# Kernel optimization log

Hardware: AMD Instinct MI355X
Metric: run time of the kernel (lower is better)

## Reference

```python
import jax, jax.numpy as jnp
import numpy as np

BLANK = 0


def setup_inputs() -> dict:
    key = jax.random.key(0)
    k1, k2 = jax.random.split(key)
    B, T, V = 64, 4096, 128
    feature = jax.random.normal(k1, (B, T, V), dtype=jnp.float32)
    lengths = jax.random.randint(k2, (B,), 1, T + 1, dtype=jnp.int32)
    return {"feature": feature, "lengths": lengths, "beam_width": 1}


def reference(feature, lengths, beam_width):
    # Greedy CTC decode (beam_width <= 1 path of the torch module), fully vectorized.
    # feature: (B, T, V) raw logits; lengths: (B,) valid frame counts.
    B, T, V = feature.shape
    logp = jax.nn.log_softmax(feature.astype(jnp.float32), axis=-1)  # (B, T, V)
    max_scores = jnp.max(logp, axis=-1)                               # (B, T)
    tokens = jnp.argmax(logp, axis=-1).astype(jnp.int32)              # (B, T)

    tmask = jnp.arange(T)[None, :] < lengths[:, None]                 # (B, T) valid frames
    logp_scores = jnp.sum(jnp.where(tmask, max_scores, 0.0), axis=-1) # (B,)

    # CTC collapse: keep token iff it is not blank and differs from previous frame's token.
    # (t != prev or prev == blank) and t != blank  ==  (t != blank) and (t != prev)
    prev = jnp.concatenate(
        [jnp.full((B, 1), BLANK, dtype=tokens.dtype), tokens[:, :-1]], axis=1
    )
    keep = (tokens != BLANK) & (tokens != prev) & tmask               # (B, T)

    # Fixed-shape encoding of the ragged prediction lists:
    # tokens[b, t] is part of prediction[b] (in time order) wherever keep[b, t].
    return tokens, keep, logp_scores
```

## Files before the change

### kernel.cpp

```cpp
#include <hip/hip_runtime.h>

#define BLANK 0

__global__ __launch_bounds__(256) void ctc_rowmax(const float* __restrict__ feat,
                                                  const int* __restrict__ lengths,
                                                  float* __restrict__ out_tok,
                                                  float* __restrict__ partial,
                                                  int npairs, int Tshift, int Tmask)
{
    const int lane = threadIdx.x & 63;
    const int l32  = lane & 31;
    const int half = lane >> 5;
    const int wid  = (blockIdx.x * 256 + (int)threadIdx.x) >> 6;
    const int nw   = (gridDim.x * 256) >> 6;
    const int nquads = npairs >> 2;

    for (int q = wid; q < nquads; q += nw) {
        const int pair0 = q << 2;
        const float4* base = (const float4*)feat + (size_t)pair0 * 64;
        float4 v0 = base[lane];
        float4 v1 = base[64 + lane];
        float4 v2 = base[128 + lane];
        float4 v3 = base[192 + lane];

        const int row0 = pair0 << 1;
        const int len  = lengths[row0 >> Tshift];
        float acc = 0.0f;

        auto process = [&](float4 v, int pair) {
            float m = v.x; int li = 0;
            if (v.y > m) { m = v.y; li = 1; }
            if (v.z > m) { m = v.z; li = 2; }
            if (v.w > m) { m = v.w; li = 3; }
            const float lm  = m;
            const int  lidx = (l32 << 2) + li;
            float s = __expf(v.x) + __expf(v.y) + __expf(v.z) + __expf(v.w);
            #pragma unroll
            for (int off = 16; off >= 1; off >>= 1) {
                m  = fmaxf(m, __shfl_xor(m, off, 64));
                s += __shfl_xor(s, off, 64);
            }
            unsigned long long bal = __ballot(lm == m);
            unsigned seg = half ? (unsigned)(bal >> 32) : (unsigned)bal;
            int src = (__ffs(seg) - 1) | (half << 5);
            int idx = __shfl(lidx, src, 64);
            const int row = (pair << 1) + half;
            if (l32 == 0) {
                out_tok[row] = (float)idx;
                if ((row & Tmask) < len) acc += m - __logf(s);
            }
        };
        process(v0, pair0);
        process(v1, pair0 + 1);
        process(v2, pair0 + 2);
        process(v3, pair0 + 3);

        acc += __shfl_xor(acc, 32, 64);
        if (lane == 0) partial[row0 >> 3] = acc;
    }
}

__global__ __launch_bounds__(256) void ctc_collapse(const int* __restrict__ lengths,
                                                    const float* __restrict__ out_tok,
                                                    const float* __restrict__ partial,
                                                    float* __restrict__ keep,
                                                    float* __restrict__ scores,
                                                    int T, int Tdiv8)
{
    const int b = blockIdx.y;
    const int t = blockIdx.x * 256 + (int)threadIdx.x;
    const size_t base = (size_t)b * T;
    if (t < T) {
        float tk = out_tok[base + t];
        float pv = (t == 0) ? (float)BLANK : out_tok[base + t - 1];
        bool valid = t < lengths[b];
        keep[base + t] = (tk != (float)BLANK && tk != pv && valid) ? 1.0f : 0.0f;
    }
    if (blockIdx.x == 0) {
        float s = 0.0f;
        for (int i = threadIdx.x; i < Tdiv8; i += 256)
            s += partial[(size_t)b * Tdiv8 + i];
        #pragma unroll
        for (int off = 32; off >= 1; off >>= 1) s += __shfl_xor(s, off, 64);
        __shared__ float red[4];
        if ((threadIdx.x & 63) == 0) red[threadIdx.x >> 6] = s;
        __syncthreads();
        if (threadIdx.x == 0) scores[b] = red[0] + red[1] + red[2] + red[3];
    }
}

extern "C" void kernel_launch(void* const* d_in, const int* in_sizes, int n_in,
                              void* d_out, int out_size, void* d_ws, size_t ws_size,
                              hipStream_t stream) {
    const float* feat    = (const float*)d_in[0];
    const int*   lengths = (const int*)d_in[1];

    const int V  = 128;
    const int B  = in_sizes[1];
    const int T  = in_sizes[0] / (B * V);
    const int BT = B * T;

    float* out_tok = (float*)d_out;
    float* keep    = out_tok + (size_t)BT;
    float* scores  = out_tok + (size_t)2 * BT;
    float* partial = (float*)d_ws;

    int Tshift = 31 - __builtin_clz((unsigned)T);
    int Tmask  = T - 1;
    int npairs = BT >> 1;

    ctc_rowmax<<<2048, 256, 0, stream>>>(feat, lengths, out_tok, partial,
                                         npairs, Tshift, Tmask);

    dim3 g2((T + 255) / 256, B);
    ctc_collapse<<<g2, 256, 0, stream>>>(lengths, out_tok, partial, keep, scores,
                                         T, T >> 3);
}
```

Baseline: 192.2 us.

## Remap rowmax so 8 lanes each own a row with 16 contiguous values

Each wavefront still handles 8 rows per iteration, but the work is now split as 8 lanes per row, each lane loading 4 consecutive float4s (16 columns), instead of one row per 32-lane half processed four times. This cuts the cross-lane reductions from four 5-step shuffle trees to a single 3-step tree, plus one ballot and index shuffle, which removes most shuffle and ballot overhead. The cost is that each lane's loads now have a 64-byte stride between lanes, so coalescing is worse than the previous fully contiguous float4 pattern. Each lane also holds more live registers.

```diff
diff --git a/kernel.cpp b/kernel.cpp
--- a/kernel.cpp
+++ b/kernel.cpp
@@ -6,57 +6,66 @@
                                                   const int* __restrict__ lengths,
                                                   float* __restrict__ out_tok,
                                                   float* __restrict__ partial,
-                                                  int npairs, int Tshift, int Tmask)
+                                                  int ngroups, int Tshift, int Tmask)
 {
     const int lane = threadIdx.x & 63;
-    const int l32  = lane & 31;
-    const int half = lane >> 5;
+    const int seg  = lane & 7;
+    const int r    = lane >> 3;
     const int wid  = (blockIdx.x * 256 + (int)threadIdx.x) >> 6;
     const int nw   = (gridDim.x * 256) >> 6;
-    const int nquads = npairs >> 2;
 
-    for (int q = wid; q < nquads; q += nw) {
-        const int pair0 = q << 2;
-        const float4* base = (const float4*)feat + (size_t)pair0 * 64;
-        float4 v0 = base[lane];
-        float4 v1 = base[64 + lane];
-        float4 v2 = base[128 + lane];
-        float4 v3 = base[192 + lane];
+    for (int g = wid; g < ngroups; g += nw) {
+        const float4* p = (const float4*)feat + ((size_t)g << 8) + (lane << 2);
+        float4 a = p[0], b = p[1], c = p[2], d = p[3];
 
-        const int row0 = pair0 << 1;
+        const int row0 = g << 3;
         const int len  = lengths[row0 >> Tshift];
+
+        const int col0 = seg << 4;
+        float m = a.x; int li = 0;
+        if (a.y > m) { m = a.y; li = 1; }
+        if (a.z > m) { m = a.z; li = 2; }
+        if (a.w > m) { m = a.w; li = 3; }
+        if (b.x > m) { m = b.x; li = 4; }
+        if (b.y > m) { m = b.y; li = 5; }
+        if (b.z > m) { m = b.z; li = 6; }
+        if (b.w > m) { m = b.w; li = 7; }
+        if (c.x > m) { m = c.x; li = 8; }
+        if (c.y > m) { m = c.y; li = 9; }
+        if (c.z > m) { m = c.z; li = 10; }
+        if (c.w > m) { m = c.w; li = 11; }
+        if (d.x > m) { m = d.x; li = 12; }
+        if (d.y > m) { m = d.y; li = 13; }
+        if (d.z > m) { m = d.z; li = 14; }
+        if (d.w > m) { m = d.w; li = 15; }
+        const float lm   = m;
+        const int   lidx = col0 + li;
+
+        float s = __expf(a.x) + __expf(a.y) + __expf(a.z) + __expf(a.w)
+                + __expf(b.x) + __expf(b.y) + __expf(b.z) + __expf(b.w)
+                + __expf(c.x) + __expf(c.y) + __expf(c.z) + __expf(c.w)
+                + __expf(d.x) + __expf(d.y) + __expf(d.z) + __expf(d.w);
+
+        #pragma unroll
+        for (int off = 4; off >= 1; off >>= 1) {
+            m  = fmaxf(m, __shfl_xor(m, off, 64));
+            s += __shfl_xor(s, off, 64);
+        }
+
+        unsigned long long bal = __ballot(lm == m);
+        int segbase = lane & ~7;
+        unsigned sb = (unsigned)((bal >> segbase) & 0xFFULL);
+        int src = segbase + __ffs(sb) - 1;
+        int idx = __shfl(lidx, src, 64);
+
         float acc = 0.0f;
-
-        auto process = [&](float4 v, int pair) {
-            float m = v.x; int li = 0;
-            if (v.y > m) { m = v.y; li = 1; }
-            if (v.z > m) { m = v.z; li = 2; }
-            if (v.w > m) { m = v.w; li = 3; }
-            const float lm  = m;
-            const int  lidx = (l32 << 2) + li;
-            float s = __expf(v.x) + __expf(v.y) + __expf(v.z) + __expf(v.w);
-            #pragma unroll
-            for (int off = 16; off >= 1; off >>= 1) {
-                m  = fmaxf(m, __shfl_xor(m, off, 64));
-                s += __shfl_xor(s, off, 64);
-            }
-            unsigned long long bal = __ballot(lm == m);
-            unsigned seg = half ? (unsigned)(bal >> 32) : (unsigned)bal;
-            int src = (__ffs(seg) - 1) | (half << 5);
-            int idx = __shfl(lidx, src, 64);
-            const int row = (pair << 1) + half;
-            if (l32 == 0) {
-                out_tok[row] = (float)idx;
-                if ((row & Tmask) < len) acc += m - __logf(s);
-            }
-        };
-        process(v0, pair0);
-        process(v1, pair0 + 1);
-        process(v2, pair0 + 2);
-        process(v3, pair0 + 3);
-
-        acc += __shfl_xor(acc, 32, 64);
-        if (lane == 0) partial[row0 >> 3] = acc;
+        if (seg == 0) {
+            out_tok[row0 + r] = (float)idx;
+            if (((row0 + r) & Tmask) < len) acc = m - __logf(s);
+        }
+        #pragma unroll
+        for (int off = 8; off <= 32; off <<= 1) acc += __shfl_xor(acc, off, 64);
+        if (lane == 0) partial[g] = acc;
     }
 }
 
@@ -107,10 +116,10 @@
 
     int Tshift = 31 - __builtin_clz((unsigned)T);
     int Tmask  = T - 1;
-    int npairs = BT >> 1;
+    int ngroups = BT >> 3;
 
     ctc_rowmax<<<2048, 256, 0, stream>>>(feat, lengths, out_tok, partial,
-                                         npairs, Tshift, Tmask);
+                                         ngroups, Tshift, Tmask);
 
     dim3 g2((T + 255) / 256, B);
     ctc_collapse<<<g2, 256, 0, stream>>>(lengths, out_tok, partial, keep, scores,
```

Result: no change. 192.5 us (+0.1%).
